# Performance work log

Hardware: AMD Instinct MI355X
Metric: run time of the kernel (lower is better)

The kernel has to match this reference:

```python
import math
import jax, jax.numpy as jnp
import numpy as np

N_HEADS = 8

def setup_inputs() -> dict:
    key = jax.random.key(0)
    qkv = jax.random.normal(key, (4, 3 * N_HEADS * 64, 2048), dtype=jnp.float32)
    return {"qkv": qkv}

def reference(qkv) -> jnp.ndarray:
    bs, width, length = qkv.shape
    assert width % (3 * N_HEADS) == 0
    ch = width // (3 * N_HEADS)
    q, k, v = jnp.split(qkv, 3, axis=1)            # each [N, H*C, T]
    scale = 1.0 / math.sqrt(math.sqrt(ch))
    qh = (q * scale).reshape(bs * N_HEADS, ch, length)  # [BH, C, T]
    kh = (k * scale).reshape(bs * N_HEADS, ch, length)
    vh = v.reshape(bs * N_HEADS, ch, length)
    weight = jnp.einsum('bct,bcs->bts', qh, kh)    # [BH, T, T]
    weight = jax.nn.softmax(weight.astype(jnp.float32), axis=-1).astype(weight.dtype)
    a = jnp.einsum('bts,bcs->bct', weight, vh)     # [BH, C, T]
    return a.reshape(bs, -1, length)
```

## Files before the change

kernel.cpp:

```cpp
#include <hip/hip_runtime.h>

#define T_LEN 2048
#define CH 64
#define NH 8
#define STILE 64
#define TTILE 256
#define WT 32
#define NIT (T_LEN / STILE)
#define KSZ (STILE * CH)
#define CS 72
#define QS 260
#define RS 68

#define QSCALE 0.180336880972948929f

typedef __attribute__((ext_vector_type(4))) float  f32x4;
typedef __attribute__((ext_vector_type(8))) __bf16 bf16x8;
typedef __attribute__((ext_vector_type(4))) __bf16 bf16x4;
typedef __attribute__((ext_vector_type(2))) __bf16 bf16x2;
typedef __attribute__((ext_vector_type(2))) unsigned int uint2v;
typedef __attribute__((ext_vector_type(4))) unsigned int uint4v;

union SMem {
  float qstage[CH * QS];
  struct {
    __bf16 k_hi[2][KSZ];
    __bf16 v_s [2][CH * CS];
  } loop;
  struct {
    float o[8][WT][RS];
    float l[2][8][4][16];
  } red;
};

#define MFMA(A, B, C) __builtin_amdgcn_mfma_f32_16x16x32_bf16((A), (B), (C), 0, 0, 0)

__device__ __forceinline__ unsigned pkbf2(float lo, float hi) {
  bf16x2 t = {(__bf16)lo, (__bf16)hi};
  return __builtin_bit_cast(unsigned, t);
}

__device__ __forceinline__ void load_k8(const float* kp, int s0, int stid, float (&kr)[8]) {
  int s  = stid & 63;
  int cg = stid >> 6;
  const float* kc = kp + (size_t)(8 * cg) * T_LEN + s0 + s;
#pragma unroll
  for (int j = 0; j < 8; ++j)
    kr[j] = kc[(size_t)j * T_LEN];
}

__device__ __forceinline__ void store_k8(__bf16* kh, int stid, const float (&kr)[8]) {
  int s  = stid & 63;
  int cg = stid >> 6;
  bf16x8 w;
#pragma unroll
  for (int j = 0; j < 8; ++j) w[j] = (__bf16)kr[j];
  int e = (s << 6) + (cg << 3);
  *(bf16x8*)&kh[e ^ ((s & 7) << 3)] = w;
}

__device__ __forceinline__ void load_v(const float* vp, int s0, int ltid, f32x4 (&vreg)[2]) {
#pragma unroll
  for (int rr = 0; rr < 2; ++rr) {
    int fidx = rr * 512 + ltid;
    int c  = fidx >> 4;
    int s4 = (fidx & 15) << 2;
    vreg[rr] = *(const f32x4*)(vp + (size_t)c * T_LEN + s0 + s4);
  }
}

__device__ __forceinline__ void store_v(__bf16* vs, int ltid, const f32x4 (&vreg)[2]) {
#pragma unroll
  for (int rr = 0; rr < 2; ++rr) {
    int fidx = rr * 512 + ltid;
    int c  = fidx >> 4;
    int s4 = (fidx & 15) << 2;
    bf16x4 vv = {(__bf16)vreg[rr].x, (__bf16)vreg[rr].y,
                 (__bf16)vreg[rr].z, (__bf16)vreg[rr].w};
    *(bf16x4*)&vs[c * CS + s4] = vv;
  }
}

__global__ __launch_bounds__(1024, 4)
void qkv_attn_mfma(const float* __restrict__ qkv, float* __restrict__ out) {
  __shared__ SMem sm;
  const int tid  = threadIdx.x;
  const int lane = tid & 63;
  const int wave = tid >> 6;
  const int wt   = wave & 7;
  const int ws   = wave >> 3;
  const int tn   = lane & 15;
  const int quad = lane >> 4;
  const int stid = tid & 511;

  const int d0 = blockIdx.x;
  const int w  = ((d0 & 7) << 5) | (d0 >> 3);
  const int ttile = w & 7;
  const int bh    = w >> 3;
  const int b = bh >> 3, h = bh & 7;
  const size_t base = (size_t)b * (3 * NH * CH) * T_LEN;
  const float* qp = qkv + base + (size_t)(CH * h) * T_LEN;
  const float* kp = qkv + base + (size_t)(CH * (NH + h)) * T_LEN;
  const float* vp = qkv + base + (size_t)(CH * (2 * NH + h)) * T_LEN;
  const int t0 = ttile * TTILE;

#pragma unroll
  for (int rr = 0; rr < 4; ++rr) {
    int fidx = rr * 1024 + tid;
    int c  = fidx >> 6;
    int t4 = (fidx & 63) << 2;
    f32x4 q4 = *(const f32x4*)(qp + (size_t)c * T_LEN + t0 + t4);
    *(f32x4*)&sm.qstage[c * QS + t4] = q4;
  }
  __syncthreads();

  bf16x8 qh[2][2];
#pragma unroll
  for (int nb = 0; nb < 2; ++nb)
#pragma unroll
    for (int kb = 0; kb < 2; ++kb) {
      int tloc = wt * WT + nb * 16 + tn;
      bf16x8 H;
#pragma unroll
      for (int j = 0; j < 8; ++j) {
        float qv = sm.qstage[(kb * 32 + quad * 8 + j) * QS + tloc] * QSCALE;
        H[j] = (__bf16)qv;
      }
      qh[nb][kb] = H;
    }
  __syncthreads();

  f32x4 acc[4][2];
  f32x4 acc_l[2];
#pragma unroll
  for (int mbc = 0; mbc < 4; ++mbc)
#pragma unroll
    for (int nb = 0; nb < 2; ++nb)
      acc[mbc][nb] = (f32x4){0.f, 0.f, 0.f, 0.f};
  acc_l[0] = (f32x4){0.f, 0.f, 0.f, 0.f};
  acc_l[1] = (f32x4){0.f, 0.f, 0.f, 0.f};

  bf16x8 av_one;
#pragma unroll
  for (int j = 0; j < 8; ++j) av_one[j] = (__bf16)1.0f;

  float  kreg[8];
  f32x4  vreg[2];
  if (ws == 0) { load_k8(kp, 0, stid, kreg); store_k8(sm.loop.k_hi[0], stid, kreg); }
  else         { load_v (vp, 0, stid, vreg); store_v (sm.loop.v_s[0], stid, vreg); }
  __syncthreads();

  for (int it = 0; it < NIT; ++it) {
    const int cur = it & 1;
    const bool more = (it + 1 < NIT);

    if (more) {
      if (ws == 0) load_k8(kp, (it + 1) * STILE, stid, kreg);
      else         load_v (vp, (it + 1) * STILE, stid, vreg);
    }

    const __bf16* kh = sm.loop.k_hi[cur];
    const int swz = (tn & 7) << 3;
    bf16x8 ah[2][2];
#pragma unroll
    for (int mb = 0; mb < 2; ++mb) {
      const int srow = 32 * ws + 16 * mb + tn;
#pragma unroll
      for (int kb = 0; kb < 2; ++kb) {
        int e = (srow << 6) + 32 * kb + 8 * quad;
        ah[mb][kb] = *(const bf16x8*)&kh[e ^ swz];
      }
    }
    f32x4 d[2][2];
#pragma unroll
    for (int mb = 0; mb < 2; ++mb)
#pragma unroll
      for (int nb = 0; nb < 2; ++nb) {
        f32x4 t = (f32x4){0.f, 0.f, 0.f, 0.f};
        t = MFMA(ah[mb][0], qh[nb][0], t);
        t = MFMA(ah[mb][1], qh[nb][1], t);
        d[mb][nb] = t;
      }

    const __bf16* vs = sm.loop.v_s[cur];
    bf16x8 av[4];
#pragma unroll
    for (int mbc = 0; mbc < 4; ++mbc)
      av[mbc] = *(const bf16x8*)&vs[(16 * mbc + tn) * CS + 32 * ws + quad * 8];

    bf16x8 bp[2];
#pragma unroll
    for (int nb = 0; nb < 2; ++nb) {
#pragma unroll
      for (int mb = 0; mb < 2; ++mb)
#pragma unroll
        for (int r = 0; r < 4; ++r)
          d[mb][nb][r] = __builtin_amdgcn_exp2f(d[mb][nb][r]);
      unsigned u00 = pkbf2(d[0][nb][0], d[0][nb][1]);
      unsigned u01 = pkbf2(d[0][nb][2], d[0][nb][3]);
      unsigned u10 = pkbf2(d[1][nb][0], d[1][nb][1]);
      unsigned u11 = pkbf2(d[1][nb][2], d[1][nb][3]);
      uint2v s0 = __builtin_amdgcn_permlane32_swap(u00, u10, false, false);
      uint2v r0 = __builtin_amdgcn_permlane16_swap(s0.x, s0.y, false, false);
      uint2v s1 = __builtin_amdgcn_permlane32_swap(u01, u11, false, false);
      uint2v r1 = __builtin_amdgcn_permlane16_swap(s1.x, s1.y, false, false);
      uint4v wv = {r0.x, r1.x, r0.y, r1.y};
      bp[nb] = __builtin_bit_cast(bf16x8, wv);
    }

#pragma unroll
    for (int mbc = 0; mbc < 4; ++mbc)
#pragma unroll
      for (int nb = 0; nb < 2; ++nb)
        acc[mbc][nb] = MFMA(av[mbc], bp[nb], acc[mbc][nb]);
#pragma unroll
    for (int nb = 0; nb < 2; ++nb)
      acc_l[nb] = MFMA(av_one, bp[nb], acc_l[nb]);

    if (more) {
      if (ws == 0) store_k8(sm.loop.k_hi[cur ^ 1], stid, kreg);
      else         store_v (sm.loop.v_s [cur ^ 1], stid, vreg);
    }
    __syncthreads();
  }

  float l_part[2] = {acc_l[0][0], acc_l[1][0]};

  if (ws == 1) {
#pragma unroll
    for (int nb = 0; nb < 2; ++nb) {
      sm.red.l[nb][wt][quad][tn] = l_part[nb];
#pragma unroll
      for (int mbc = 0; mbc < 4; ++mbc)
        *(f32x4*)&sm.red.o[wt][nb * 16 + tn][16 * mbc + quad * 4] = acc[mbc][nb];
    }
  }
  __syncthreads();
  if (ws == 0) {
    float* op = out + (size_t)bh * CH * T_LEN;
#pragma unroll
    for (int nb = 0; nb < 2; ++nb) {
      float l = l_part[nb] + sm.red.l[nb][wt][quad][tn];
      float inv_l = 1.0f / l;
      int t = t0 + wt * WT + nb * 16 + tn;
#pragma unroll
      for (int mbc = 0; mbc < 4; ++mbc) {
        f32x4 o = acc[mbc][nb] + *(const f32x4*)&sm.red.o[wt][nb * 16 + tn][16 * mbc + quad * 4];
        o = o * inv_l;
        int c = 16 * mbc + quad * 4;
        op[(size_t)(c + 0) * T_LEN + t] = o.x;
        op[(size_t)(c + 1) * T_LEN + t] = o.y;
        op[(size_t)(c + 2) * T_LEN + t] = o.z;
        op[(size_t)(c + 3) * T_LEN + t] = o.w;
      }
    }
  }
}

extern "C" void kernel_launch(void* const* d_in, const int* in_sizes, int n_in,
                              void* d_out, int out_size, void* d_ws, size_t ws_size,
                              hipStream_t stream) {
  const float* qkv = (const float*)d_in[0];
  float* out = (float*)d_out;
  dim3 grid(256);
  qkv_attn_mfma<<<grid, 1024, 0, stream>>>(qkv, out);
}
```

Measured before the change: 117.1 us.

## Process two K/V tiles per barrier with a four-slot LDS ring

```diff
diff --git a/kernel.cpp b/kernel.cpp
--- a/kernel.cpp
+++ b/kernel.cpp
@@ -24,8 +24,8 @@
 union SMem {
   float qstage[CH * QS];
   struct {
-    __bf16 k_hi[2][KSZ];
-    __bf16 v_s [2][CH * CS];
+    __bf16 k_hi[4][KSZ];
+    __bf16 v_s [4][CH * CS];
   } loop;
   struct {
     float o[8][WT][RS];
@@ -40,44 +40,42 @@
   return __builtin_bit_cast(unsigned, t);
 }
 
-__device__ __forceinline__ void load_k8(const float* kp, int s0, int stid, float (&kr)[8]) {
+__device__ __forceinline__ bf16x8 load_k8_cvt(const float* kp, int s0, int stid) {
   int s  = stid & 63;
   int cg = stid >> 6;
   const float* kc = kp + (size_t)(8 * cg) * T_LEN + s0 + s;
+  bf16x8 w;
 #pragma unroll
   for (int j = 0; j < 8; ++j)
-    kr[j] = kc[(size_t)j * T_LEN];
-}
-
-__device__ __forceinline__ void store_k8(__bf16* kh, int stid, const float (&kr)[8]) {
+    w[j] = (__bf16)kc[(size_t)j * T_LEN];
+  return w;
+}
+
+__device__ __forceinline__ void store_k8w(__bf16* kh, int stid, bf16x8 w) {
   int s  = stid & 63;
   int cg = stid >> 6;
-  bf16x8 w;
-#pragma unroll
-  for (int j = 0; j < 8; ++j) w[j] = (__bf16)kr[j];
   int e = (s << 6) + (cg << 3);
   *(bf16x8*)&kh[e ^ ((s & 7) << 3)] = w;
 }
 
-__device__ __forceinline__ void load_v(const float* vp, int s0, int ltid, f32x4 (&vreg)[2]) {
+__device__ __forceinline__ void load_v_cvt(const float* vp, int s0, int ltid, bf16x4 (&vv)[2]) {
 #pragma unroll
   for (int rr = 0; rr < 2; ++rr) {
     int fidx = rr * 512 + ltid;
     int c  = fidx >> 4;
     int s4 = (fidx & 15) << 2;
-    vreg[rr] = *(const f32x4*)(vp + (size_t)c * T_LEN + s0 + s4);
-  }
-}
-
-__device__ __forceinline__ void store_v(__bf16* vs, int ltid, const f32x4 (&vreg)[2]) {
+    f32x4 t = *(const f32x4*)(vp + (size_t)c * T_LEN + s0 + s4);
+    vv[rr] = (bf16x4){(__bf16)t.x, (__bf16)t.y, (__bf16)t.z, (__bf16)t.w};
+  }
+}
+
+__device__ __forceinline__ void store_vw(__bf16* vs, int ltid, const bf16x4 (&vv)[2]) {
 #pragma unroll
   for (int rr = 0; rr < 2; ++rr) {
     int fidx = rr * 512 + ltid;
     int c  = fidx >> 4;
     int s4 = (fidx & 15) << 2;
-    bf16x4 vv = {(__bf16)vreg[rr].x, (__bf16)vreg[rr].y,
-                 (__bf16)vreg[rr].z, (__bf16)vreg[rr].w};
-    *(bf16x4*)&vs[c * CS + s4] = vv;
+    *(bf16x4*)&vs[c * CS + s4] = vv[rr];
   }
 }
 
@@ -102,14 +100,14 @@
   const float* qp = qkv + base + (size_t)(CH * h) * T_LEN;
   const float* kp = qkv + base + (size_t)(CH * (NH + h)) * T_LEN;
   const float* vp = qkv + base + (size_t)(CH * (2 * NH + h)) * T_LEN;
-  const int t0 = ttile * TTILE;
+  const int t0q = ttile * TTILE;
 
 #pragma unroll
   for (int rr = 0; rr < 4; ++rr) {
     int fidx = rr * 1024 + tid;
     int c  = fidx >> 6;
     int t4 = (fidx & 63) << 2;
-    f32x4 q4 = *(const f32x4*)(qp + (size_t)c * T_LEN + t0 + t4);
+    f32x4 q4 = *(const f32x4*)(qp + (size_t)c * T_LEN + t0q + t4);
     *(f32x4*)&sm.qstage[c * QS + t4] = q4;
   }
   __syncthreads();
@@ -144,22 +142,9 @@
 #pragma unroll
   for (int j = 0; j < 8; ++j) av_one[j] = (__bf16)1.0f;
 
-  float  kreg[8];
-  f32x4  vreg[2];
-  if (ws == 0) { load_k8(kp, 0, stid, kreg); store_k8(sm.loop.k_hi[0], stid, kreg); }
-  else         { load_v (vp, 0, stid, vreg); store_v (sm.loop.v_s[0], stid, vreg); }
-  __syncthreads();
-
-  for (int it = 0; it < NIT; ++it) {
-    const int cur = it & 1;
-    const bool more = (it + 1 < NIT);
-
-    if (more) {
-      if (ws == 0) load_k8(kp, (it + 1) * STILE, stid, kreg);
-      else         load_v (vp, (it + 1) * STILE, stid, vreg);
-    }
-
-    const __bf16* kh = sm.loop.k_hi[cur];
+  auto body = [&](int bi) {
+    const __bf16* kh = sm.loop.k_hi[bi];
+    const __bf16* vs = sm.loop.v_s[bi];
     const int swz = (tn & 7) << 3;
     bf16x8 ah[2][2];
 #pragma unroll
@@ -182,7 +167,6 @@
         d[mb][nb] = t;
       }
 
-    const __bf16* vs = sm.loop.v_s[cur];
     bf16x8 av[4];
 #pragma unroll
     for (int mbc = 0; mbc < 4; ++mbc)
@@ -216,10 +200,49 @@
 #pragma unroll
     for (int nb = 0; nb < 2; ++nb)
       acc_l[nb] = MFMA(av_one, bp[nb], acc_l[nb]);
+  };
+
+  bf16x8 kbA, kbB;
+  bf16x4 vvA[2], vvB[2];
+  if (ws == 0) {
+    kbA = load_k8_cvt(kp, 0,     stid);
+    kbB = load_k8_cvt(kp, STILE, stid);
+    store_k8w(sm.loop.k_hi[0], stid, kbA);
+    store_k8w(sm.loop.k_hi[1], stid, kbB);
+  } else {
+    load_v_cvt(vp, 0,     stid, vvA);
+    load_v_cvt(vp, STILE, stid, vvB);
+    store_vw(sm.loop.v_s[0], stid, vvA);
+    store_vw(sm.loop.v_s[1], stid, vvB);
+  }
+  __syncthreads();
+
+  for (int p = 0; p < NIT / 2; ++p) {
+    const int t0 = 2 * p;
+    const bool more = (p + 1 < NIT / 2);
 
     if (more) {
-      if (ws == 0) store_k8(sm.loop.k_hi[cur ^ 1], stid, kreg);
-      else         store_v (sm.loop.v_s [cur ^ 1], stid, vreg);
+      if (ws == 0) {
+        kbA = load_k8_cvt(kp, (t0 + 2) * STILE, stid);
+        kbB = load_k8_cvt(kp, (t0 + 3) * STILE, stid);
+      } else {
+        load_v_cvt(vp, (t0 + 2) * STILE, stid, vvA);
+        load_v_cvt(vp, (t0 + 3) * STILE, stid, vvB);
+      }
+    }
+
+    body(t0 & 3);
+
+    if (more) {
+      if (ws == 0) store_k8w(sm.loop.k_hi[(t0 + 2) & 3], stid, kbA);
+      else         store_vw (sm.loop.v_s [(t0 + 2) & 3], stid, vvA);
+    }
+
+    body((t0 + 1) & 3);
+
+    if (more) {
+      if (ws == 0) store_k8w(sm.loop.k_hi[(t0 + 3) & 3], stid, kbB);
+      else         store_vw (sm.loop.v_s [(t0 + 3) & 3], stid, vvB);
     }
     __syncthreads();
   }
@@ -242,7 +265,7 @@
     for (int nb = 0; nb < 2; ++nb) {
       float l = l_part[nb] + sm.red.l[nb][wt][quad][tn];
       float inv_l = 1.0f / l;
-      int t = t0 + wt * WT + nb * 16 + tn;
+      int t = t0q + wt * WT + nb * 16 + tn;
 #pragma unroll
       for (int mbc = 0; mbc < 4; ++mbc) {
         f32x4 o = acc[mbc][nb] + *(const f32x4*)&sm.red.o[wt][nb * 16 + tn][16 * mbc + quad * 4];
```

Result: slower. 126.8 us (+8.2%).
